# Kernel optimization log

Hardware: AMD Instinct MI355X
Metric: run time of the kernel (lower is better)

Reference implementation:

```python
import jax, jax.numpy as jnp
import numpy as np

DIM = 1024
HEADS = 16
DIM_HEAD = 64
INNER = HEADS * DIM_HEAD  # 1024
EPS = 1e-5


def layernorm(x, w, b):
    mu = jnp.mean(x, axis=-1, keepdims=True)
    var = jnp.mean(jnp.square(x - mu), axis=-1, keepdims=True)
    return (x - mu) * jax.lax.rsqrt(var + EPS) * w + b


def setup_inputs() -> dict:
    key = jax.random.key(0)
    ks = jax.random.split(key, 9)
    b, n1, n2 = 4, 4096, 256
    x = jax.random.normal(ks[0], (b, n1, DIM), dtype=jnp.float32)
    latents = jax.random.normal(ks[1], (b, n2, DIM), dtype=jnp.float32)
    shift = jax.random.normal(ks[2], (b, HEADS), dtype=jnp.float32)
    scale = jax.random.normal(ks[3], (b, HEADS), dtype=jnp.float32)
    s = 1.0 / np.sqrt(DIM)
    Wq = jax.random.normal(ks[4], (DIM, INNER), dtype=jnp.float32) * s
    Wkv = jax.random.normal(ks[5], (DIM, 2 * INNER), dtype=jnp.float32) * s
    Wout = jax.random.normal(ks[6], (INNER, DIM), dtype=jnp.float32) * (1.0 / np.sqrt(INNER))
    ln1_w = jnp.ones((DIM,), jnp.float32)
    ln1_b = jnp.zeros((DIM,), jnp.float32)
    ln2_w = jnp.ones((DIM,), jnp.float32)
    ln2_b = jnp.zeros((DIM,), jnp.float32)
    return {"x": x, "latents": latents, "shift": shift, "scale": scale,
            "ln1_w": ln1_w, "ln1_b": ln1_b, "ln2_w": ln2_w, "ln2_b": ln2_b,
            "Wq": Wq, "Wkv": Wkv, "Wout": Wout}


def reference(x, latents, shift, scale, ln1_w, ln1_b, ln2_w, ln2_b, Wq, Wkv, Wout):
    b = x.shape[0]
    xn = layernorm(x, ln1_w, ln1_b)            # (b, n1, D)
    ln = layernorm(latents, ln2_w, ln2_b)      # (b, n2, D)
    q = ln @ Wq                                 # (b, n2, inner)
    kv = xn @ Wkv                               # (b, n1, 2*inner)
    k, v = jnp.split(kv, 2, axis=-1)
    q = q.reshape(b, -1, HEADS, DIM_HEAD)
    k = k.reshape(b, -1, HEADS, DIM_HEAD)
    v = v.reshape(b, -1, HEADS, DIM_HEAD)
    # AdaLN-style per-head modulation on q
    q = q * (1.0 + scale[:, None, :, None]) + shift[:, None, :, None]
    # fp32 attention scores (already fp32 here)
    attn_scale = DIM_HEAD ** -0.5
    qk = jnp.einsum('bihd,bjhd->bhij', q.astype(jnp.float32), k.astype(jnp.float32)) * attn_scale
    attn = jax.nn.softmax(qk, axis=-1).astype(v.dtype)  # (b, h, n2, n1)
    out = jnp.einsum('bhij,bjhd->bihd', attn, v)         # (b, n2, h, dh)
    out = out.reshape(b, -1, INNER)
    return out @ Wout
```

## Files before the change

### kernel.cpp

```cpp
#include <hip/hip_runtime.h>

typedef __bf16 bf16;
typedef bf16 bf16x8 __attribute__((ext_vector_type(8)));
typedef bf16 bf16x4 __attribute__((ext_vector_type(4)));
typedef float f32x4 __attribute__((ext_vector_type(4)));

#define B_ 4
#define N1 4096
#define N2 256
#define DIM 1024
#define HEADS 16
#define DH 64
#define INNER 1024
#define ASPLIT 4
#define KEYS_PER_SPLIT (N1 / ASPLIT)
#define SPLIT_ELEMS (4 * 16 * 256 * 64)
#define ROWS_TOTAL (4 * HEADS * N2)

typedef __attribute__((address_space(1))) const void gvoid_t;
typedef __attribute__((address_space(3))) void lvoid_t;
__device__ __forceinline__ void async16(const void* g, void* l) {
  __builtin_amdgcn_global_load_lds((gvoid_t*)g, (lvoid_t*)l, 16, 0, 0);
}

__global__ __launch_bounds__(256) void prep(
    const float* __restrict__ Wq, const float* __restrict__ Wkv,
    const float* __restrict__ Wout, bf16* __restrict__ WqT,
    bf16* __restrict__ WkvT, bf16* __restrict__ WoutT,
    const float* __restrict__ x, const float* __restrict__ latents,
    const float* __restrict__ ln1w, const float* __restrict__ ln1b,
    const float* __restrict__ ln2w, const float* __restrict__ ln2b,
    bf16* __restrict__ xn, bf16* __restrict__ lnl) {
  __shared__ float tile[32][33];
  int t = blockIdx.x;
  if (t < 4096) {
    const float* src;
    bf16* dst;
    int N;
    if (t < 1024) { src = Wq; dst = WqT; N = 1024; }
    else if (t < 3072) { t -= 1024; src = Wkv; dst = WkvT; N = 2048; }
    else { t -= 3072; src = Wout; dst = WoutT; N = 1024; }
    int ntiles = N >> 5;
    int n0 = (t % ntiles) * 32, k0 = (t / ntiles) * 32;
    int xx = threadIdx.x & 31, yy = threadIdx.x >> 5;
    for (int j = 0; j < 4; j++)
      tile[yy + 8 * j][xx] = src[(size_t)(k0 + yy + 8 * j) * N + n0 + xx];
    __syncthreads();
    for (int j = 0; j < 4; j++)
      dst[(size_t)(n0 + yy + 8 * j) * 1024 + k0 + xx] = (bf16)tile[xx][yy + 8 * j];
    return;
  }
  int wv = threadIdx.x >> 6, lane = threadIdx.x & 63;
  int grow = (t - 4096) * 4 + wv;
  const float *src, *w, *bb;
  bf16* dst;
  int row;
  if (grow < 16384) { src = x; w = ln1w; bb = ln1b; dst = xn; row = grow; }
  else { src = latents; w = ln2w; bb = ln2b; dst = lnl; row = grow - 16384; }
  const float4* p = (const float4*)(src + (size_t)row * DIM);
  float4 v[4];
  for (int j = 0; j < 4; j++) v[j] = p[j * 64 + lane];
  float s = 0.f, sq = 0.f;
  for (int j = 0; j < 4; j++) {
    s += v[j].x + v[j].y + v[j].z + v[j].w;
    sq += v[j].x * v[j].x + v[j].y * v[j].y + v[j].z * v[j].z + v[j].w * v[j].w;
  }
  for (int off = 32; off; off >>= 1) {
    s += __shfl_xor(s, off, 64);
    sq += __shfl_xor(sq, off, 64);
  }
  float mu = s * (1.0f / DIM);
  float var = sq * (1.0f / DIM) - mu * mu;
  float r = rsqrtf(var + 1e-5f);
  for (int j = 0; j < 4; j++) {
    float4 wv4 = ((const float4*)w)[j * 64 + lane];
    float4 bv4 = ((const float4*)bb)[j * 64 + lane];
    bf16x4 o;
    o[0] = (bf16)((v[j].x - mu) * r * wv4.x + bv4.x);
    o[1] = (bf16)((v[j].y - mu) * r * wv4.y + bv4.y);
    o[2] = (bf16)((v[j].z - mu) * r * wv4.z + bv4.z);
    o[3] = (bf16)((v[j].w - mu) * r * wv4.w + bv4.w);
    *(bf16x4*)(dst + (size_t)row * DIM + (j * 64 + lane) * 4) = o;
  }
}

__device__ __forceinline__ int swz_off(int row, int cb) {
  int line = row >> 1;
  return (line << 7) + (((((row & 1) << 2) | cb) ^ (line & 7)) << 4);
}

__global__ __launch_bounds__(512, 2) void gemm_kv256(
    const bf16* __restrict__ A, const bf16* __restrict__ Bt,
    bf16* __restrict__ Cout, bf16* __restrict__ Cout2) {
  extern __shared__ char smem[];
  int tid = threadIdx.x;
  int lane = tid & 63, wv = tid >> 6;
  int lr = lane & 15, quad = lane >> 4;
  int wr = wv >> 2, wc = wv & 3;
  int bid = blockIdx.x;
  int mt = (bid & 7) * 8 + ((bid >> 3) >> 3), nt = (bid >> 3) & 7;
  int m0 = mt * 256, n0 = nt * 256;

  int offA[8], offB[4];
#pragma unroll
  for (int im = 0; im < 8; im++) offA[im] = swz_off(wr * 128 + im * 16 + lr, quad);
#pragma unroll
  for (int in = 0; in < 4; in++) offB[in] = swz_off(wc * 64 + in * 16 + lr, quad);

  size_t gA[2], gB[2];
#pragma unroll
  for (int s = 0; s < 2; s++) {
    int u = s * 512 + tid;
    int line = u >> 3, inner = (u & 7) ^ (line & 7);
    int row = line * 2 + (inner >> 2), cb = inner & 3;
    gA[s] = (size_t)(m0 + row) * 1024 + cb * 8;
    gB[s] = (size_t)(n0 + row) * 1024 + cb * 8;
  }
  int ldsS0 = wv * 1024, ldsS1 = 8192 + wv * 1024;

  auto stA = [&](int b, int kh, int k0) {
    char* base = smem + b * 32768 + kh * 16384;
    async16(&A[gA[0] + k0], base + ldsS0);
    async16(&A[gA[1] + k0], base + ldsS1);
  };
  auto stB = [&](int b, int kh, int k0) {
    char* base = smem + 65536 + b * 32768 + kh * 16384;
    async16(&Bt[gB[0] + k0], base + ldsS0);
    async16(&Bt[gB[1] + k0], base + ldsS1);
  };

  f32x4 acc[8][4] = {};

  stA(0, 0, 0);  stB(0, 0, 0);
  stA(0, 1, 32); stB(0, 1, 32);
  stA(1, 0, 64); stB(1, 0, 64);
  asm volatile("s_waitcnt vmcnt(4)" ::: "memory");
  __builtin_amdgcn_s_barrier();

#pragma unroll 1
  for (int t = 0; t < 16; t++) {
    int b = t & 1;
    const char* A0 = smem + b * 32768;
    const char* A1 = A0 + 16384;
    const char* B0 = smem + 65536 + b * 32768;
    const char* B1 = B0 + 16384;
    int k1 = (t + 1 < 16 ? t + 1 : 15) * 64;
    int k2 = (t + 2 < 16 ? t + 2 : 15) * 64;
    bf16x8 af[4], bfr[4];
#pragma unroll
    for (int in = 0; in < 4; in++) bfr[in] = *(const bf16x8*)(B0 + offB[in]);
#pragma unroll
    for (int im = 0; im < 4; im++) af[im] = *(const bf16x8*)(A0 + offA[im]);
    stA(b ^ 1, 1, k1 + 32);
    __builtin_amdgcn_s_barrier();
    __builtin_amdgcn_s_setprio(1);
#pragma unroll
    for (int im = 0; im < 4; im++)
#pragma unroll
      for (int in = 0; in < 4; in++)
        acc[im][in] = __builtin_amdgcn_mfma_f32_16x16x32_bf16(
            af[im], bfr[in], acc[im][in], 0, 0, 0);
    __builtin_amdgcn_s_setprio(0);
    __builtin_amdgcn_s_barrier();
#pragma unroll
    for (int im = 0; im < 4; im++) af[im] = *(const bf16x8*)(A0 + offA[4 + im]);
    stB(b ^ 1, 1, k1 + 32);
    __builtin_amdgcn_s_barrier();
    __builtin_amdgcn_s_setprio(1);
#pragma unroll
    for (int im = 0; im < 4; im++)
#pragma unroll
      for (int in = 0; in < 4; in++)
        acc[4 + im][in] = __builtin_amdgcn_mfma_f32_16x16x32_bf16(
            af[im], bfr[in], acc[4 + im][in], 0, 0, 0);
    __builtin_amdgcn_s_setprio(0);
    __builtin_amdgcn_s_barrier();
#pragma unroll
    for (int in = 0; in < 4; in++) bfr[in] = *(const bf16x8*)(B1 + offB[in]);
#pragma unroll
    for (int im = 0; im < 4; im++) af[im] = *(const bf16x8*)(A1 + offA[im]);
    stA(b, 0, k2);
    __builtin_amdgcn_s_barrier();
    __builtin_amdgcn_s_setprio(1);
#pragma unroll
    for (int im = 0; im < 4; im++)
#pragma unroll
      for (int in = 0; in < 4; in++)
        acc[im][in] = __builtin_amdgcn_mfma_f32_16x16x32_bf16(
            af[im], bfr[in], acc[im][in], 0, 0, 0);
    __builtin_amdgcn_s_setprio(0);
    __builtin_amdgcn_s_barrier();
#pragma unroll
    for (int im = 0; im < 4; im++) af[im] = *(const bf16x8*)(A1 + offA[4 + im]);
    stB(b, 0, k2);
    __builtin_amdgcn_s_barrier();
    __builtin_amdgcn_s_setprio(1);
#pragma unroll
    for (int im = 0; im < 4; im++)
#pragma unroll
      for (int in = 0; in < 4; in++)
        acc[4 + im][in] = __builtin_amdgcn_mfma_f32_16x16x32_bf16(
            af[im], bfr[in], acc[4 + im][in], 0, 0, 0);
    __builtin_amdgcn_s_setprio(0);
    asm volatile("s_waitcnt vmcnt(4)" ::: "memory");
    __builtin_amdgcn_s_barrier();
  }

  asm volatile("s_waitcnt vmcnt(0)" ::: "memory");
  __builtin_amdgcn_s_barrier();

  if (n0 < 1024) {
#pragma unroll
    for (int im = 0; im < 8; im++)
#pragma unroll
      for (int in = 0; in < 4; in++) {
        int col = n0 + wc * 64 + in * 16 + lr;
#pragma unroll
        for (int r = 0; r < 4; r++) {
          int row = m0 + wr * 128 + im * 16 + quad * 4 + r;
          Cout[(size_t)row * 1024 + col] = (bf16)acc[im][in][r];
        }
      }
    return;
  }
  int b2 = m0 >> 12;
  int key0 = (m0 & 4095) + wr * 128;
  int gc0 = (n0 - 1024) + wc * 64;
  bf16* Tw = (bf16*)(smem + wv * 8704);
  for (int pass = 0; pass < 2; pass++) {
#pragma unroll
    for (int ii = 0; ii < 2; ii++) {
      int in = pass * 2 + ii;
      int cl = ii * 16 + lr;
#pragma unroll
      for (int im = 0; im < 8; im++) {
        bf16x4 pk;
#pragma unroll
        for (int r = 0; r < 4; r++) pk[r] = (bf16)acc[im][in][r];
        *(bf16x4*)&Tw[cl * 136 + im * 16 + quad * 4] = pk;
      }
    }
    asm volatile("s_waitcnt lgkmcnt(0)" ::: "memory");
#pragma unroll
    for (int j = 0; j < 8; j++) {
      int idx = j * 64 + lane;
      int cl = idx >> 4, k8 = idx & 15;
      uint4 val = *(const uint4*)&Tw[cl * 136 + k8 * 8];
      *(uint4*)&Cout2[((size_t)(b2 * 1024 + gc0 + pass * 32 + cl)) * 4096 +
                      key0 + k8 * 8] = val;
    }
    asm volatile("s_waitcnt lgkmcnt(0)" ::: "memory");
  }
}

template <int MODE>
__global__ __launch_bounds__(256) void gemm64(
    const bf16* __restrict__ A, const bf16* __restrict__ Bt,
    void* __restrict__ Cout, int K, int N,
    const float* __restrict__ shiftp, const float* __restrict__ scalep) {
  __shared__ __align__(16) bf16 As[64 * 64];
  __shared__ __align__(16) bf16 Bs[64 * 64];
  int tid = threadIdx.x;
  int lane = tid & 63, wv = tid >> 6;
  int wr = wv >> 1, wc = wv & 1;
  int quad = lane >> 4, lr = lane & 15;
  int m0 = blockIdx.y * 64, n0 = blockIdx.x * 64;
  f32x4 acc[2][2] = {};
  for (int kt = 0; kt < K; kt += 64) {
    __syncthreads();
    for (int j = 0; j < 2; j++) {
      int idx0 = j * 256 + wv * 64;
      int row = (idx0 >> 3) + (lane >> 3);
      int cb = (lane & 7) ^ (row & 7);
      async16(&A[(size_t)(m0 + row) * K + kt + cb * 8], &As[idx0 * 8]);
      async16(&Bt[(size_t)(n0 + row) * K + kt + cb * 8], &Bs[idx0 * 8]);
    }
    __syncthreads();
    for (int kk = 0; kk < 2; kk++) {
      bf16x8 af[2], bfr[2];
      for (int im = 0; im < 2; im++) {
        int row = wr * 32 + im * 16 + lr;
        af[im] = *(const bf16x8*)&As[row * 64 + ((quad + 4 * kk) ^ (row & 7)) * 8];
      }
      for (int in = 0; in < 2; in++) {
        int row = wc * 32 + in * 16 + lr;
        bfr[in] = *(const bf16x8*)&Bs[row * 64 + ((quad + 4 * kk) ^ (row & 7)) * 8];
      }
      for (int im = 0; im < 2; im++)
        for (int in = 0; in < 2; in++)
          acc[im][in] = __builtin_amdgcn_mfma_f32_16x16x32_bf16(
              af[im], bfr[in], acc[im][in], 0, 0, 0);
    }
  }
  for (int im = 0; im < 2; im++)
    for (int in = 0; in < 2; in++) {
      int col = n0 + wc * 32 + in * 16 + lr;
      for (int r = 0; r < 4; r++) {
        int row = m0 + wr * 32 + im * 16 + quad * 4 + r;
        float v = acc[im][in][r];
        if (MODE == 1) {
          int bb = row >> 8, hh = col >> 6;
          float sc = scalep[bb * 16 + hh], sh = shiftp[bb * 16 + hh];
          ((bf16*)Cout)[(size_t)row * N + col] =
              (bf16)((v * (1.0f + sc) + sh) * 0.18033688011112042f);
        } else {
          ((float*)Cout)[(size_t)row * N + col] = v;
        }
      }
    }
}

__global__ __launch_bounds__(256) void attn_kernel(const bf16* __restrict__ q,
                                                   const bf16* __restrict__ kb,
                                                   const bf16* __restrict__ vt,
                                                   bf16* __restrict__ opb,
                                                   float* __restrict__ lseb) {
  int b = blockIdx.z, h = blockIdx.y;
  int qp = blockIdx.x >> 2, sp = blockIdx.x & 3;
  int tid = threadIdx.x, lane = tid & 63, wv = tid >> 6;
  int quad = lane >> 4, lr = lane & 15;
  __shared__ __align__(16) bf16 Ks[64 * 64];
  __shared__ __align__(16) bf16 Vs[64 * 64];
  __shared__ __align__(16) bf16 QP[128 * 64];
  __shared__ float abuf[4][16];
  int q0 = qp * 128;

  const bf16* qg = q + (size_t)(b * N2 + q0) * INNER + h * DH;
  for (int j = 0; j < 4; j++) {
    int r0 = j * 32 + wv * 8;
    int r = r0 + (lane >> 3);
    async16(&qg[(size_t)r * INNER + ((lane & 7) ^ (r & 7)) * 8], &QP[r0 * 64]);
  }
  __syncthreads();
  bf16x8 aQ[2][2];
  for (int g = 0; g < 2; g++) {
    int row = wv * 32 + g * 16 + lr;
    for (int kk = 0; kk < 2; kk++)
      aQ[g][kk] = *(const bf16x8*)&QP[row * 64 + ((quad + 4 * kk) ^ (row & 7)) * 8];
  }
  float m_s[2] = {-1e30f, -1e30f}, l_s[2] = {0.0f, 0.0f};
  f32x4 oacc[2][4] = {};

  const bf16* kg = kb + (size_t)(b * N1) * 1024 + h * DH;
  const bf16* vg = vt + (size_t)((b * HEADS + h) * DH) * N1;
  bf16* Ps = QP + wv * 2048;

  for (int t = 0; t < KEYS_PER_SPLIT / 64; t++) {
    int key0 = sp * KEYS_PER_SPLIT + t * 64;
    __syncthreads();
    for (int j = 0; j < 2; j++) {
      int r0 = j * 32 + wv * 8;
      int r = r0 + (lane >> 3);
      int cs = ((lane & 7) ^ (r & 7)) * 8;
      async16(&kg[(size_t)(key0 + r) * 1024 + cs], &Ks[r0 * 64]);
      async16(&vg[(size_t)r * N1 + key0 + cs], &Vs[r0 * 64]);
    }
    __syncthreads();

    bf16x8 ak[2][4], bv[2][4];
    for (int kk = 0; kk < 2; kk++)
      for (int nt = 0; nt < 4; nt++) {
        int row = nt * 16 + lr;
        ak[kk][nt] =
            *(const bf16x8*)&Ks[row * 64 + ((quad + 4 * kk) ^ (row & 7)) * 8];
        bv[kk][nt] =
            *(const bf16x8*)&Vs[row * 64 + ((quad + 4 * kk) ^ (row & 7)) * 8];
      }

    for (int g = 0; g < 2; g++) {
      f32x4 s[4] = {};
      for (int kk = 0; kk < 2; kk++)
        for (int nt = 0; nt < 4; nt++)
          s[nt] = __builtin_amdgcn_mfma_f32_16x16x32_bf16(ak[kk][nt], aQ[g][kk],
                                                          s[nt], 0, 0, 0);
      float mx = s[0][0];
      for (int nt = 0; nt < 4; nt++)
        for (int r = 0; r < 4; r++) mx = fmaxf(mx, s[nt][r]);
      mx = fmaxf(mx, __shfl_xor(mx, 16, 64));
      mx = fmaxf(mx, __shfl_xor(mx, 32, 64));
      float mn = fmaxf(m_s[g], mx);
      float al = exp2f(m_s[g] - mn);
      float p[4][4], sum = 0.0f;
      for (int nt = 0; nt < 4; nt++)
        for (int r = 0; r < 4; r++) {
          p[nt][r] = exp2f(s[nt][r] - mn);
          sum += p[nt][r];
        }
      sum += __shfl_xor(sum, 16, 64);
      sum += __shfl_xor(sum, 32, 64);
      l_s[g] = l_s[g] * al + sum;
      m_s[g] = mn;
      if (quad == 0) abuf[wv][lr] = al;

      for (int nt = 0; nt < 4; nt++) {
        bf16x4 pk;
        for (int r = 0; r < 4; r++) pk[r] = (bf16)p[nt][r];
        *(bf16x4*)&Ps[lr * 64 + ((2 * nt + (quad >> 1)) ^ (lr & 7)) * 8 +
                      (quad & 1) * 4] = pk;
      }

      f32x4 a4 = *(const f32x4*)&abuf[wv][quad * 4];
      for (int in = 0; in < 4; in++)
        for (int r = 0; r < 4; r++) oacc[g][in][r] *= a4[r];

      bf16x8 aP[2];
      for (int kk = 0; kk < 2; kk++)
        aP[kk] = *(const bf16x8*)&Ps[lr * 64 + ((4 * kk + quad) ^ (lr & 7)) * 8];
      for (int kk = 0; kk < 2; kk++)
        for (int in = 0; in < 4; in++)
          oacc[g][in] = __builtin_amdgcn_mfma_f32_16x16x32_bf16(
              aP[kk], bv[kk][in], oacc[g][in], 0, 0, 0);
    }
  }

  bf16* ob = opb + (size_t)sp * SPLIT_ELEMS;
  size_t rbase = (size_t)(b * HEADS + h) * N2;
  for (int g = 0; g < 2; g++) {
    for (int r = 0; r < 4; r++) {
      float lrow = __shfl(l_s[g], quad * 4 + r, 16);
      float inv = 1.0f / lrow;
      int qq = q0 + wv * 32 + g * 16 + quad * 4 + r;
      for (int in = 0; in < 4; in++)
        ob[(rbase + qq) * 64 + in * 16 + lr] = (bf16)(oacc[g][in][r] * inv);
    }
    if (quad == 0) {
      int qq = q0 + wv * 32 + g * 16 + lr;
      lseb[(size_t)sp * ROWS_TOTAL + rbase + qq] = m_s[g] + __log2f(l_s[g]);
    }
  }
}

__global__ __launch_bounds__(256) void combine_kernel(const bf16* __restrict__ opb,
                                                      const float* __restrict__ lseb,
                                                      bf16* __restrict__ out) {
  int gid = blockIdx.x * 256 + threadIdx.x;
  int d = gid & 63;
  int rq = gid >> 6;
  int qq = rq & 255, bh = rq >> 8;
  int h = bh & 15, b = bh >> 4;
  float ls[ASPLIT];
  for (int s = 0; s < ASPLIT; s++) ls[s] = lseb[(size_t)s * ROWS_TOTAL + rq];
  float M = fmaxf(fmaxf(ls[0], ls[1]), fmaxf(ls[2], ls[3]));
  float L = 0.0f, o = 0.0f;
  for (int s = 0; s < ASPLIT; s++) {
    float w = exp2f(ls[s] - M);
    L += w;
    o += w * (float)opb[(size_t)s * SPLIT_ELEMS + (size_t)rq * 64 + d];
  }
  out[((size_t)(b * N2 + qq)) * INNER + h * DH + d] = (bf16)(o / L);
}

extern "C" void kernel_launch(void* const* d_in, const int* in_sizes, int n_in,
                              void* d_out, int out_size, void* d_ws,
                              size_t ws_size, hipStream_t stream) {
  const float* x       = (const float*)d_in[0];
  const float* latents = (const float*)d_in[1];
  const float* shift   = (const float*)d_in[2];
  const float* scale   = (const float*)d_in[3];
  const float* ln1w    = (const float*)d_in[4];
  const float* ln1b    = (const float*)d_in[5];
  const float* ln2w    = (const float*)d_in[6];
  const float* ln2b    = (const float*)d_in[7];
  const float* Wq      = (const float*)d_in[8];
  const float* Wkv     = (const float*)d_in[9];
  const float* Wout    = (const float*)d_in[10];

  char* ws = (char*)d_ws;
  bf16*  xn    = (bf16*)(ws);
  bf16*  opb   = (bf16*)(ws);
  bf16*  lnl   = (bf16*)(ws + 33554432);
  float* lseb  = (float*)(ws + 33554432);
  bf16*  qb    = (bf16*)(ws + 35651584);
  bf16*  kb    = (bf16*)(ws + 37748736);
  bf16*  vtb   = (bf16*)(ws + 104857600);
  bf16*  aob   = (bf16*)(ws + 138412032);
  bf16*  WqT   = (bf16*)(ws + 140509184);
  bf16*  WkvT  = (bf16*)(ws + 142606336);
  bf16*  WoutT = (bf16*)(ws + 146800640);

  static bool attr_done = false;
  if (!attr_done) {
    hipFuncSetAttribute(reinterpret_cast<const void*>(gemm_kv256),
                        hipFuncAttributeMaxDynamicSharedMemorySize, 131072);
    attr_done = true;
  }

  prep<<<8448, 256, 0, stream>>>(Wq, Wkv, Wout, WqT, WkvT, WoutT, x, latents,
                                 ln1w, ln1b, ln2w, ln2b, xn, lnl);
  gemm_kv256<<<dim3(512), dim3(512), 131072, stream>>>(xn, WkvT, kb, vtb);
  gemm64<1><<<dim3(16, 16), 256, 0, stream>>>(lnl, WqT, qb, 1024, 1024, shift,
                                              scale);
  attn_kernel<<<dim3(2 * ASPLIT, 16, 4), 256, 0, stream>>>(qb, kb, vtb, opb,
                                                           lseb);
  combine_kernel<<<16384, 256, 0, stream>>>(opb, lseb, aob);
  gemm64<2><<<dim3(16, 16), 256, 0, stream>>>(aob, WoutT, d_out, 1024, 1024,
                                              nullptr, nullptr);
}
```

Baseline: 275.8 us.

## Persistent two-tile KV GEMM and double-buffered K/V staging in attention

Measured after the change: 314.4 us. +14.0%, slower.

```diff
diff --git a/kernel.cpp b/kernel.cpp
--- a/kernel.cpp
+++ b/kernel.cpp
@@ -89,6 +89,12 @@
   return (line << 7) + (((((row & 1) << 2) | cb) ^ (line & 7)) << 4);
 }
 
+#define MFMA_BLOCK(base)                                              \
+  _Pragma("unroll") for (int im = 0; im < 4; im++)                    \
+      _Pragma("unroll") for (int in = 0; in < 4; in++)                \
+          acc[(base) + im][in] = __builtin_amdgcn_mfma_f32_16x16x32_bf16( \
+              af[im], bfr[in], acc[(base) + im][in], 0, 0, 0);
+
 __global__ __launch_bounds__(512, 2) void gemm_kv256(
     const bf16* __restrict__ A, const bf16* __restrict__ Bt,
     bf16* __restrict__ Cout, bf16* __restrict__ Cout2) {
@@ -98,7 +104,9 @@
   int lr = lane & 15, quad = lane >> 4;
   int wr = wv >> 2, wc = wv & 3;
   int bid = blockIdx.x;
-  int mt = (bid & 7) * 8 + ((bid >> 3) >> 3), nt = (bid >> 3) & 7;
+  int xcd = bid & 7, idx = bid >> 3;
+  int mt = xcd * 4 + (idx & 3);
+  int nt = idx >> 2;
   int m0 = mt * 256, n0 = nt * 256;
 
   int offA[8], offB[4];
@@ -118,139 +126,112 @@
   }
   int ldsS0 = wv * 1024, ldsS1 = 8192 + wv * 1024;
 
-  auto stA = [&](int b, int kh, int k0) {
+  auto stA = [&](int b, int kh, int w) {
     char* base = smem + b * 32768 + kh * 16384;
+    size_t k0 = (size_t)((w & 15) * 64 + kh * 32) +
+                (w >= 16 ? (size_t)8192 * 1024 : 0);
     async16(&A[gA[0] + k0], base + ldsS0);
     async16(&A[gA[1] + k0], base + ldsS1);
   };
-  auto stB = [&](int b, int kh, int k0) {
+  auto stB = [&](int b, int kh, int w) {
     char* base = smem + 65536 + b * 32768 + kh * 16384;
+    size_t k0 = (size_t)((w & 15) * 64 + kh * 32);
     async16(&Bt[gB[0] + k0], base + ldsS0);
     async16(&Bt[gB[1] + k0], base + ldsS1);
   };
 
   f32x4 acc[8][4] = {};
 
+  auto storeC = [&](int mbase) {
+    if (n0 < 1024) {
+#pragma unroll
+      for (int im = 0; im < 8; im++)
+#pragma unroll
+        for (int in = 0; in < 4; in++) {
+          int col = n0 + wc * 64 + in * 16 + lr;
+#pragma unroll
+          for (int r = 0; r < 4; r++) {
+            int row = mbase + wr * 128 + im * 16 + quad * 4 + r;
+            Cout[(size_t)row * 1024 + col] = (bf16)acc[im][in][r];
+          }
+        }
+    } else {
+      int b2 = mbase >> 12;
+      int key0 = (mbase & 4095) + wr * 128;
+      int c0 = (n0 - 1024) + wc * 64;
+#pragma unroll
+      for (int im = 0; im < 8; im++)
+#pragma unroll
+        for (int in = 0; in < 4; in++) {
+          bf16x4 pk;
+#pragma unroll
+          for (int r = 0; r < 4; r++) pk[r] = (bf16)acc[im][in][r];
+          *(bf16x4*)&Cout2[((size_t)(b2 * 1024 + c0 + in * 16 + lr)) * 4096 +
+                           key0 + im * 16 + quad * 4] = pk;
+        }
+    }
+  };
+
   stA(0, 0, 0);  stB(0, 0, 0);
-  stA(0, 1, 32); stB(0, 1, 32);
-  stA(1, 0, 64); stB(1, 0, 64);
+  stA(0, 1, 0);  stB(0, 1, 0);
+  stA(1, 0, 1);  stB(1, 0, 1);
   asm volatile("s_waitcnt vmcnt(4)" ::: "memory");
   __builtin_amdgcn_s_barrier();
 
 #pragma unroll 1
-  for (int t = 0; t < 16; t++) {
-    int b = t & 1;
+  for (int u = 0; u < 32; u++) {
+    int b = u & 1;
     const char* A0 = smem + b * 32768;
     const char* A1 = A0 + 16384;
     const char* B0 = smem + 65536 + b * 32768;
     const char* B1 = B0 + 16384;
-    int k1 = (t + 1 < 16 ? t + 1 : 15) * 64;
-    int k2 = (t + 2 < 16 ? t + 2 : 15) * 64;
+    int w1 = (u + 1 < 32) ? u + 1 : 31;
+    int w2 = (u + 2 < 32) ? u + 2 : 31;
     bf16x8 af[4], bfr[4];
 #pragma unroll
     for (int in = 0; in < 4; in++) bfr[in] = *(const bf16x8*)(B0 + offB[in]);
 #pragma unroll
     for (int im = 0; im < 4; im++) af[im] = *(const bf16x8*)(A0 + offA[im]);
-    stA(b ^ 1, 1, k1 + 32);
+    stA(b ^ 1, 1, w1);
     __builtin_amdgcn_s_barrier();
     __builtin_amdgcn_s_setprio(1);
-#pragma unroll
-    for (int im = 0; im < 4; im++)
-#pragma unroll
-      for (int in = 0; in < 4; in++)
-        acc[im][in] = __builtin_amdgcn_mfma_f32_16x16x32_bf16(
-            af[im], bfr[in], acc[im][in], 0, 0, 0);
+    MFMA_BLOCK(0)
     __builtin_amdgcn_s_setprio(0);
-    __builtin_amdgcn_s_barrier();
 #pragma unroll
     for (int im = 0; im < 4; im++) af[im] = *(const bf16x8*)(A0 + offA[4 + im]);
-    stB(b ^ 1, 1, k1 + 32);
+    stB(b ^ 1, 1, w1);
     __builtin_amdgcn_s_barrier();
     __builtin_amdgcn_s_setprio(1);
-#pragma unroll
-    for (int im = 0; im < 4; im++)
-#pragma unroll
-      for (int in = 0; in < 4; in++)
-        acc[4 + im][in] = __builtin_amdgcn_mfma_f32_16x16x32_bf16(
-            af[im], bfr[in], acc[4 + im][in], 0, 0, 0);
+    MFMA_BLOCK(4)
     __builtin_amdgcn_s_setprio(0);
     __builtin_amdgcn_s_barrier();
 #pragma unroll
     for (int in = 0; in < 4; in++) bfr[in] = *(const bf16x8*)(B1 + offB[in]);
 #pragma unroll
     for (int im = 0; im < 4; im++) af[im] = *(const bf16x8*)(A1 + offA[im]);
-    stA(b, 0, k2);
+    stA(b, 0, w2);
     __builtin_amdgcn_s_barrier();
     __builtin_amdgcn_s_setprio(1);
-#pragma unroll
-    for (int im = 0; im < 4; im++)
-#pragma unroll
-      for (int in = 0; in < 4; in++)
-        acc[im][in] = __builtin_amdgcn_mfma_f32_16x16x32_bf16(
-            af[im], bfr[in], acc[im][in], 0, 0, 0);
+    MFMA_BLOCK(0)
     __builtin_amdgcn_s_setprio(0);
-    __builtin_amdgcn_s_barrier();
 #pragma unroll
     for (int im = 0; im < 4; im++) af[im] = *(const bf16x8*)(A1 + offA[4 + im]);
-    stB(b, 0, k2);
+    stB(b, 0, w2);
     __builtin_amdgcn_s_barrier();
     __builtin_amdgcn_s_setprio(1);
-#pragma unroll
-    for (int im = 0; im < 4; im++)
-#pragma unroll
-      for (int in = 0; in < 4; in++)
-        acc[4 + im][in] = __builtin_amdgcn_mfma_f32_16x16x32_bf16(
-            af[im], bfr[in], acc[4 + im][in], 0, 0, 0);
+    MFMA_BLOCK(4)
     __builtin_amdgcn_s_setprio(0);
     asm volatile("s_waitcnt vmcnt(4)" ::: "memory");
     __builtin_amdgcn_s_barrier();
-  }
-
-  asm volatile("s_waitcnt vmcnt(0)" ::: "memory");
-  __builtin_amdgcn_s_barrier();
-
-  if (n0 < 1024) {
-#pragma unroll
-    for (int im = 0; im < 8; im++)
-#pragma unroll
-      for (int in = 0; in < 4; in++) {
-        int col = n0 + wc * 64 + in * 16 + lr;
-#pragma unroll
-        for (int r = 0; r < 4; r++) {
-          int row = m0 + wr * 128 + im * 16 + quad * 4 + r;
-          Cout[(size_t)row * 1024 + col] = (bf16)acc[im][in][r];
-        }
-      }
-    return;
-  }
-  int b2 = m0 >> 12;
-  int key0 = (m0 & 4095) + wr * 128;
-  int gc0 = (n0 - 1024) + wc * 64;
-  bf16* Tw = (bf16*)(smem + wv * 8704);
-  for (int pass = 0; pass < 2; pass++) {
-#pragma unroll
-    for (int ii = 0; ii < 2; ii++) {
-      int in = pass * 2 + ii;
-      int cl = ii * 16 + lr;
-#pragma unroll
-      for (int im = 0; im < 8; im++) {
-        bf16x4 pk;
-#pragma unroll
-        for (int r = 0; r < 4; r++) pk[r] = (bf16)acc[im][in][r];
-        *(bf16x4*)&Tw[cl * 136 + im * 16 + quad * 4] = pk;
-      }
-    }
-    asm volatile("s_waitcnt lgkmcnt(0)" ::: "memory");
-#pragma unroll
-    for (int j = 0; j < 8; j++) {
-      int idx = j * 64 + lane;
-      int cl = idx >> 4, k8 = idx & 15;
-      uint4 val = *(const uint4*)&Tw[cl * 136 + k8 * 8];
-      *(uint4*)&Cout2[((size_t)(b2 * 1024 + gc0 + pass * 32 + cl)) * 4096 +
-                      key0 + k8 * 8] = val;
-    }
-    asm volatile("s_waitcnt lgkmcnt(0)" ::: "memory");
-  }
+    if (u == 15) {
+      storeC(m0);
+#pragma unroll
+      for (int im = 0; im < 8; im++)
+#pragma unroll
+        for (int in = 0; in < 4; in++) acc[im][in] = (f32x4){0.f, 0.f, 0.f, 0.f};
+    }
+  }
+  storeC(m0 + 8192);
 }
 
 template <int MODE>
@@ -319,8 +300,8 @@
   int qp = blockIdx.x >> 2, sp = blockIdx.x & 3;
   int tid = threadIdx.x, lane = tid & 63, wv = tid >> 6;
   int quad = lane >> 4, lr = lane & 15;
-  __shared__ __align__(16) bf16 Ks[64 * 64];
-  __shared__ __align__(16) bf16 Vs[64 * 64];
+  __shared__ __align__(16) bf16 Ks[2][64 * 64];
+  __shared__ __align__(16) bf16 Vs[2][64 * 64];
   __shared__ __align__(16) bf16 QP[128 * 64];
   __shared__ float abuf[4][16];
   int q0 = qp * 128;
@@ -345,27 +326,33 @@
   const bf16* vg = vt + (size_t)((b * HEADS + h) * DH) * N1;
   bf16* Ps = QP + wv * 2048;
 
-  for (int t = 0; t < KEYS_PER_SPLIT / 64; t++) {
+  auto stageKV = [&](int t, int buf) {
     int key0 = sp * KEYS_PER_SPLIT + t * 64;
-    __syncthreads();
     for (int j = 0; j < 2; j++) {
       int r0 = j * 32 + wv * 8;
       int r = r0 + (lane >> 3);
       int cs = ((lane & 7) ^ (r & 7)) * 8;
-      async16(&kg[(size_t)(key0 + r) * 1024 + cs], &Ks[r0 * 64]);
-      async16(&vg[(size_t)r * N1 + key0 + cs], &Vs[r0 * 64]);
-    }
-    __syncthreads();
-
+      async16(&kg[(size_t)(key0 + r) * 1024 + cs], &Ks[buf][r0 * 64]);
+      async16(&vg[(size_t)r * N1 + key0 + cs], &Vs[buf][r0 * 64]);
+    }
+  };
+
+  stageKV(0, 0);
+  asm volatile("s_waitcnt vmcnt(0)" ::: "memory");
+  __builtin_amdgcn_s_barrier();
+
+  for (int t = 0; t < KEYS_PER_SPLIT / 64; t++) {
+    int cur = t & 1;
     bf16x8 ak[2][4], bv[2][4];
     for (int kk = 0; kk < 2; kk++)
       for (int nt = 0; nt < 4; nt++) {
         int row = nt * 16 + lr;
         ak[kk][nt] =
-            *(const bf16x8*)&Ks[row * 64 + ((quad + 4 * kk) ^ (row & 7)) * 8];
+            *(const bf16x8*)&Ks[cur][row * 64 + ((quad + 4 * kk) ^ (row & 7)) * 8];
         bv[kk][nt] =
-            *(const bf16x8*)&Vs[row * 64 + ((quad + 4 * kk) ^ (row & 7)) * 8];
+            *(const bf16x8*)&Vs[cur][row * 64 + ((quad + 4 * kk) ^ (row & 7)) * 8];
       }
+    if (t + 1 < KEYS_PER_SPLIT / 64) stageKV(t + 1, cur ^ 1);
 
     for (int g = 0; g < 2; g++) {
       f32x4 s[4] = {};
@@ -411,6 +398,8 @@
           oacc[g][in] = __builtin_amdgcn_mfma_f32_16x16x32_bf16(
               aP[kk], bv[kk][in], oacc[g][in], 0, 0, 0);
     }
+    asm volatile("s_waitcnt vmcnt(0)" ::: "memory");
+    __builtin_amdgcn_s_barrier();
   }
 
   bf16* ob = opb + (size_t)sp * SPLIT_ELEMS;
@@ -487,7 +476,7 @@
 
   prep<<<8448, 256, 0, stream>>>(Wq, Wkv, Wout, WqT, WkvT, WoutT, x, latents,
                                  ln1w, ln1b, ln2w, ln2b, xn, lnl);
-  gemm_kv256<<<dim3(512), dim3(512), 131072, stream>>>(xn, WkvT, kb, vtb);
+  gemm_kv256<<<dim3(256), dim3(512), 131072, stream>>>(xn, WkvT, kb, vtb);
   gemm64<1><<<dim3(16, 16), 256, 0, stream>>>(lnl, WqT, qb, 1024, 1024, shift,
                                               scale);
   attn_kernel<<<dim3(2 * ASPLIT, 16, 4), 256, 0, stream>>>(qb, kb, vtb, opb,
```

## Multi-buffer LDS tiles to overlap global loads with MFMA in GEMM and attention

Applied to the files above, without the earlier changes.

Measured after the change: 278.4 us. About the same (+0.9%).

```diff
diff --git a/kernel.cpp b/kernel.cpp
--- a/kernel.cpp
+++ b/kernel.cpp
@@ -258,40 +258,58 @@
     const bf16* __restrict__ A, const bf16* __restrict__ Bt,
     void* __restrict__ Cout, int K, int N,
     const float* __restrict__ shiftp, const float* __restrict__ scalep) {
-  __shared__ __align__(16) bf16 As[64 * 64];
-  __shared__ __align__(16) bf16 Bs[64 * 64];
+  __shared__ __align__(16) bf16 As[3][64 * 64];
+  __shared__ __align__(16) bf16 Bs[3][64 * 64];
   int tid = threadIdx.x;
   int lane = tid & 63, wv = tid >> 6;
   int wr = wv >> 1, wc = wv & 1;
   int quad = lane >> 4, lr = lane & 15;
   int m0 = blockIdx.y * 64, n0 = blockIdx.x * 64;
   f32x4 acc[2][2] = {};
-  for (int kt = 0; kt < K; kt += 64) {
-    __syncthreads();
+
+  auto stage = [&](int step, int buf) {
+    int kt = step * 64;
     for (int j = 0; j < 2; j++) {
       int idx0 = j * 256 + wv * 64;
       int row = (idx0 >> 3) + (lane >> 3);
       int cb = (lane & 7) ^ (row & 7);
-      async16(&A[(size_t)(m0 + row) * K + kt + cb * 8], &As[idx0 * 8]);
-      async16(&Bt[(size_t)(n0 + row) * K + kt + cb * 8], &Bs[idx0 * 8]);
-    }
-    __syncthreads();
+      async16(&A[(size_t)(m0 + row) * K + kt + cb * 8], &As[buf][idx0 * 8]);
+      async16(&Bt[(size_t)(n0 + row) * K + kt + cb * 8], &Bs[buf][idx0 * 8]);
+    }
+  };
+
+  int nsteps = K >> 6;
+  stage(0, 0);
+  stage(1, 1);
+  asm volatile("s_waitcnt vmcnt(4)" ::: "memory");
+  __builtin_amdgcn_s_barrier();
+
+#pragma unroll 1
+  for (int s = 0; s < nsteps; s++) {
+    int cur = s % 3;
+    int nxt = (s + 2 < nsteps) ? s + 2 : nsteps - 1;
+    stage(nxt, (s + 2) % 3);
     for (int kk = 0; kk < 2; kk++) {
       bf16x8 af[2], bfr[2];
       for (int im = 0; im < 2; im++) {
         int row = wr * 32 + im * 16 + lr;
-        af[im] = *(const bf16x8*)&As[row * 64 + ((quad + 4 * kk) ^ (row & 7)) * 8];
+        af[im] =
+            *(const bf16x8*)&As[cur][row * 64 + ((quad + 4 * kk) ^ (row & 7)) * 8];
       }
       for (int in = 0; in < 2; in++) {
         int row = wc * 32 + in * 16 + lr;
-        bfr[in] = *(const bf16x8*)&Bs[row * 64 + ((quad + 4 * kk) ^ (row & 7)) * 8];
+        bfr[in] =
+            *(const bf16x8*)&Bs[cur][row * 64 + ((quad + 4 * kk) ^ (row & 7)) * 8];
       }
       for (int im = 0; im < 2; im++)
         for (int in = 0; in < 2; in++)
           acc[im][in] = __builtin_amdgcn_mfma_f32_16x16x32_bf16(
               af[im], bfr[in], acc[im][in], 0, 0, 0);
     }
-  }
+    asm volatile("s_waitcnt vmcnt(4)" ::: "memory");
+    __builtin_amdgcn_s_barrier();
+  }
+
   for (int im = 0; im < 2; im++)
     for (int in = 0; in < 2; in++) {
       int col = n0 + wc * 32 + in * 16 + lr;
@@ -319,8 +337,8 @@
   int qp = blockIdx.x >> 2, sp = blockIdx.x & 3;
   int tid = threadIdx.x, lane = tid & 63, wv = tid >> 6;
   int quad = lane >> 4, lr = lane & 15;
-  __shared__ __align__(16) bf16 Ks[64 * 64];
-  __shared__ __align__(16) bf16 Vs[64 * 64];
+  __shared__ __align__(16) bf16 Ks[2][64 * 64];
+  __shared__ __align__(16) bf16 Vs[2][64 * 64];
   __shared__ __align__(16) bf16 QP[128 * 64];
   __shared__ float abuf[4][16];
   int q0 = qp * 128;
@@ -345,27 +363,33 @@
   const bf16* vg = vt + (size_t)((b * HEADS + h) * DH) * N1;
   bf16* Ps = QP + wv * 2048;
 
-  for (int t = 0; t < KEYS_PER_SPLIT / 64; t++) {
+  auto stageKV = [&](int t, int buf) {
     int key0 = sp * KEYS_PER_SPLIT + t * 64;
-    __syncthreads();
     for (int j = 0; j < 2; j++) {
       int r0 = j * 32 + wv * 8;
       int r = r0 + (lane >> 3);
       int cs = ((lane & 7) ^ (r & 7)) * 8;
-      async16(&kg[(size_t)(key0 + r) * 1024 + cs], &Ks[r0 * 64]);
-      async16(&vg[(size_t)r * N1 + key0 + cs], &Vs[r0 * 64]);
-    }
-    __syncthreads();
-
+      async16(&kg[(size_t)(key0 + r) * 1024 + cs], &Ks[buf][r0 * 64]);
+      async16(&vg[(size_t)r * N1 + key0 + cs], &Vs[buf][r0 * 64]);
+    }
+  };
+
+  stageKV(0, 0);
+  asm volatile("s_waitcnt vmcnt(0)" ::: "memory");
+  __builtin_amdgcn_s_barrier();
+
+  for (int t = 0; t < KEYS_PER_SPLIT / 64; t++) {
+    int cur = t & 1;
     bf16x8 ak[2][4], bv[2][4];
     for (int kk = 0; kk < 2; kk++)
       for (int nt = 0; nt < 4; nt++) {
         int row = nt * 16 + lr;
         ak[kk][nt] =
-            *(const bf16x8*)&Ks[row * 64 + ((quad + 4 * kk) ^ (row & 7)) * 8];
+            *(const bf16x8*)&Ks[cur][row * 64 + ((quad + 4 * kk) ^ (row & 7)) * 8];
         bv[kk][nt] =
-            *(const bf16x8*)&Vs[row * 64 + ((quad + 4 * kk) ^ (row & 7)) * 8];
-      }
+            *(const bf16x8*)&Vs[cur][row * 64 + ((quad + 4 * kk) ^ (row & 7)) * 8];
+      }
+    if (t + 1 < KEYS_PER_SPLIT / 64) stageKV(t + 1, cur ^ 1);
 
     for (int g = 0; g < 2; g++) {
       f32x4 s[4] = {};
@@ -411,6 +435,8 @@
           oacc[g][in] = __builtin_amdgcn_mfma_f32_16x16x32_bf16(
               aP[kk], bv[kk][in], oacc[g][in], 0, 0, 0);
     }
+    asm volatile("s_waitcnt vmcnt(0)" ::: "memory");
+    __builtin_amdgcn_s_barrier();
   }
 
   bf16* ob = opb + (size_t)sp * SPLIT_ELEMS;
```
